# Kernel optimization log

Hardware: AMD Instinct MI355X
Metric: run time of the kernel (lower is better)

Reference implementation:

```python
import jax, jax.numpy as jnp
import numpy as np

LSTM = 256
NUM_CELLS = 5
BLOCKS = 6
TEMP = 5.0
TANH_C = 1.1


def setup_inputs() -> dict:
    key = jax.random.key(0)
    ks = jax.random.split(key, 8)
    s = 0.05  # small init so sigmoids/tanh stay in sane range
    return {
        "enc_w": jax.random.normal(ks[0], (5, LSTM), jnp.float32) * s,
        "w_ih": jax.random.normal(ks[1], (4 * LSTM, LSTM), jnp.float32) * s,
        "w_hh": jax.random.normal(ks[2], (4 * LSTM, LSTM), jnp.float32) * s,
        "b_ih": jax.random.normal(ks[3], (4 * LSTM,), jnp.float32) * s,
        "b_hh": jax.random.normal(ks[4], (4 * LSTM,), jnp.float32) * s,
        "w1": jax.random.normal(ks[5], (LSTM, LSTM), jnp.float32) * s,
        "w2": jax.random.normal(ks[6], (LSTM, LSTM), jnp.float32) * s,
        "v": jax.random.normal(ks[7], (LSTM,), jnp.float32) * s,
    }


def _lstm_cell(x, h, c, w_ih, w_hh, b_ih, b_hh):
    # torch.nn.LSTMCell gate order: i, f, g, o
    g = w_ih @ x + b_ih + w_hh @ h + b_hh  # [4*LSTM]
    i, f, gg, o = jnp.split(g, 4)
    i, f, o = jax.nn.sigmoid(i), jax.nn.sigmoid(f), jax.nn.sigmoid(o)
    c2 = f * c + i * jnp.tanh(gg)
    h2 = o * jnp.tanh(c2)
    return h2, c2


def _run_sampler(bkey, enc_w, w_ih, w_hh, b_ih, b_hh, w1, w2, v):
    zeros = jnp.zeros((LSTM,), jnp.float32)
    inputs = enc_w[0]  # encoder(0)
    anchors = []
    anchors_w1 = []
    prev_h = prev_c = zeros
    # first two layers: LSTM always fed zero state (faithful to source)
    for _ in range(2):
        prev_h, prev_c = _lstm_cell(inputs, zeros, zeros, w_ih, w_hh, b_ih, b_hh)
        anchors.append(zeros)
        anchors_w1.append(w1 @ prev_h)
    arc_seq, log_probs, entropies = [], [], []
    step = 0
    for layer_id in range(2, NUM_CELLS + 2):
        for _ in range(2):
            prev_h, prev_c = _lstm_cell(inputs, prev_h, prev_c, w_ih, w_hh, b_ih, b_hh)
            q = jnp.tanh(jnp.stack(anchors_w1[:layer_id]) + w2 @ prev_h)  # [layer_id, LSTM]
            logits = (q @ v) / TEMP  # [layer_id]
            logits = TANH_C * jnp.tanh(logits)
            skey = jax.random.fold_in(bkey, step); step += 1
            index = jax.random.categorical(skey, logits)
            lsm = jax.nn.log_softmax(logits)
            arc_seq.append(index)
            log_probs.append(-lsm[index])  # F.cross_entropy
            entropies.append(jax.lax.stop_gradient(-jnp.sum(lsm * jnp.exp(lsm))))
            inputs = jnp.stack(anchors[:layer_id])[index]
        prev_h, prev_c = _lstm_cell(inputs, prev_h, prev_c, w_ih, w_hh, b_ih, b_hh)
        anchors.append(prev_h)
        anchors_w1.append(w1 @ prev_h)
        inputs = enc_w[0]
    arc = jnp.stack(arc_seq)  # [2*NUM_CELLS] int
    return arc, sum(entropies), sum(log_probs), prev_c, prev_h


def reference(enc_w, w_ih, w_hh, b_ih, b_hh, w1, w2, v):
    key = jax.random.key(42)
    all_arc = []
    all_entropy = jnp.float32(0.0)
    all_log_prob = jnp.float32(0.0)
    c = h = None
    for b in range(BLOCKS):
        arc, ent, lp, c, h = _run_sampler(
            jax.random.fold_in(key, b), enc_w, w_ih, w_hh, b_ih, b_hh, w1, w2, v)
        all_arc.append(arc)
        all_entropy = all_entropy + ent
        all_log_prob = all_log_prob + lp
    return (jnp.stack(all_arc), all_log_prob, all_entropy, c[None, :], h[None, :])
```

## Files before the change

### kernel.cpp

```cpp
#include <hip/hip_runtime.h>
#include <stdint.h>


#define NBLK  6
#define PWG   8
#define THR   512
#define TINYF 1.17549435e-38f
#define HTAGB 0xC3B00000u
#define YTAGB 0xE1700000u
#define ITAGB 0xA5D00000u
#define DONE_MAGIC 0x444f4e45

typedef unsigned long long u64;
struct U2 { uint32_t x, y; };

#define W_DONE 0u
#define W_PART 32u
#define W_IDX  80u
#define W_HX   320u
#define W_YMB  24896u
#define W_NEED 221504u

#define S_READY 0u
#define S_DONE  192u
#define S_PART  224u
#define S_HP    320u
#define S_ACC   24896u
#define FXS     67108864.0f
#define READY_MAGIC 0x52454459

__device__ __forceinline__ U2 tf2x32(uint32_t k0, uint32_t k1,
                                     uint32_t c0, uint32_t c1) {
  uint32_t ks2 = k0 ^ k1 ^ 0x1BD11BDAu;
  uint32_t x0 = c0 + k0, x1 = c1 + k1;
#define TFR(r) { x0 += x1; x1 = (x1 << (r)) | (x1 >> (32 - (r))); x1 ^= x0; }
  TFR(13) TFR(15) TFR(26) TFR(6)   x0 += k1;  x1 += ks2 + 1u;
  TFR(17) TFR(29) TFR(16) TFR(24)  x0 += ks2; x1 += k0 + 2u;
  TFR(13) TFR(15) TFR(26) TFR(6)   x0 += k0;  x1 += k1 + 3u;
  TFR(17) TFR(29) TFR(16) TFR(24)  x0 += k1;  x1 += ks2 + 4u;
  TFR(13) TFR(15) TFR(26) TFR(6)   x0 += ks2; x1 += k0 + 5u;
#undef TFR
  U2 r; r.x = x0; r.y = x1; return r;
}

__device__ __forceinline__ float sigf(float x) {
  return 1.0f / (1.0f + expf(-x));
}
__device__ __forceinline__ void istore(int* p, int v) {
  __hip_atomic_store(p, v, __ATOMIC_RELAXED, __HIP_MEMORY_SCOPE_AGENT);
}
__device__ __forceinline__ int iload(const int* p) {
  return __hip_atomic_load(p, __ATOMIC_RELAXED, __HIP_MEMORY_SCOPE_AGENT);
}
__device__ __forceinline__ void hstore(u64* p, u64 v) {
  __hip_atomic_store(p, v, __ATOMIC_RELAXED, __HIP_MEMORY_SCOPE_AGENT);
}
__device__ __forceinline__ u64 hload(const u64* p) {
  return __hip_atomic_load(p, __ATOMIC_RELAXED, __HIP_MEMORY_SCOPE_AGENT);
}
__device__ __forceinline__ void fstore(float* p, float v) {
  __hip_atomic_store(p, v, __ATOMIC_RELAXED, __HIP_MEMORY_SCOPE_AGENT);
}
__device__ __forceinline__ float fload(const float* p) {
  return __hip_atomic_load(p, __ATOMIC_RELAXED, __HIP_MEMORY_SCOPE_AGENT);
}
__device__ __forceinline__ u64 pollw(const u64* p, uint32_t want) {
  u64 v;
  for (;;) {
    v = hload(p);
    if ((uint32_t)(v >> 32) == want) return v;
    __builtin_amdgcn_s_sleep(1);
  }
}

__global__ __launch_bounds__(THR, 2) void ctrl_v16(
    const float* __restrict__ enc_w,
    const float* __restrict__ wih,
    const float* __restrict__ whh,
    const float* __restrict__ b_ih,
    const float* __restrict__ b_hh,
    const float* __restrict__ w1,
    const float* __restrict__ w2,
    const float* __restrict__ vvec,
    unsigned char* __restrict__ ws,
    float* __restrict__ out) {

  const int b = blockIdx.x & 7;
  const int p = blockIdx.x >> 3;
  if (b >= NBLK) return;
  const int tid = threadIdx.x;

  int*   done = (int*)(ws + W_DONE);
  float* part = (float*)(ws + W_PART);
  int*   idxw = (int*)(ws + W_IDX);
  u64*   hx   = (u64*)(ws + W_HX);
  u64*   ymb  = (u64*)(ws + W_YMB);

  const int rl = tid & 127, s = tid >> 7;
  const int grow = (rl >> 5) * 256 + p * 32 + (rl & 31);
  const int k0 = s * 64;
  const int rr = tid & 255, ks = tid >> 8;
  const int cb = p * 32 + ks * 16;

  __shared__ __align__(16) float gateL[THR];
  __shared__ __align__(16) float hL[256], encL[256], vL[256];
  __shared__ __align__(16) float anchL[4][256];
  __shared__ __align__(16) float w2hS[256], aw1S[6][256];
  __shared__ float rowSumL[128], biasS[128], h2S[32];
  __shared__ float logitL[8];
  __shared__ int   selL;

  if (tid < 256) { encL[tid] = enc_w[tid]; vL[tid] = vvec[tid]; }
  if (tid < 128) {
    int r = (tid >> 5) * 256 + p * 32 + (tid & 31);
    biasS[tid] = b_ih[r] + b_hh[r];
  }

  float4 wihr[16], whhr[16];
  #pragma unroll
  for (int c = 0; c < 16; ++c) {
    wihr[c] = *(const float4*)(wih + grow * 256 + k0 + c * 4);
    whhr[c] = *(const float4*)(whh + grow * 256 + k0 + c * 4);
  }
  float w1c[16], w2c[16];
  #pragma unroll
  for (int j = 0; j < 16; ++j) {
    w1c[j] = w1[rr * 256 + cb + j];
    w2c[j] = w2[rr * 256 + cb + j];
  }
  __syncthreads();

  auto dotIH = [&](const float* x) {
    float a = 0.0f;
    #pragma unroll
    for (int c = 0; c < 16; ++c) {
      float4 xv = *(const float4*)(x + k0 + c * 4);
      float4 w = wihr[c];
      a += w.x * xv.x + w.y * xv.y + w.z * xv.z + w.w * xv.w;
    }
    return a;
  };
  auto dotHH = [&]() {
    float a = 0.0f;
    #pragma unroll
    for (int c = 0; c < 16; ++c) {
      float4 xv = *(const float4*)(hL + k0 + c * 4);
      float4 w = whhr[c];
      a += w.x * xv.x + w.y * xv.y + w.z * xv.z + w.w * xv.w;
    }
    return a;
  };

  const float encih = dotIH(encL);

  float cv = 0.0f;
  U2 bk = tf2x32(0u, 42u, 0u, (uint32_t)b);
  int k = 1, step = 0;
  float lpAcc = 0.0f, entAcc = 0.0f;

  auto cell = [&](float gacc, int mode, int aid, int cid) {
    gateL[tid] = gacc;
    __syncthreads();
    if (tid < 128) {
      float ssum = 0.0f;
      #pragma unroll
      for (int j = 0; j < 4; ++j) ssum += gateL[j * 128 + tid];
      rowSumL[tid] = ssum + biasS[tid];
    }
    __syncthreads();
    if (tid < 32) {
      float gi = rowSumL[tid],       gf = rowSumL[32 + tid];
      float gg2 = rowSumL[64 + tid], go = rowSumL[96 + tid];
      float c2 = sigf(gf) * cv + sigf(gi) * tanhf(gg2);
      float h2 = sigf(go) * tanhf(c2);
      cv = c2;
      h2S[tid] = h2;
      if (mode == 2) {
        if (b == NBLK - 1) { out[62 + p * 32 + tid] = cv; out[318 + p * 32 + tid] = h2; }
      } else {
        hstore(&hx[(k & 1) * 1536 + b * 256 + p * 32 + tid],
               ((u64)(HTAGB | (uint32_t)k) << 32) | (u64)__float_as_uint(h2));
      }
    }
    __syncthreads();
    if (mode == 2) return;

    {
      const float* wc = (mode == 1) ? w1c : w2c;
      float yp = 0.0f;
      #pragma unroll
      for (int j = 0; j < 16; ++j) yp += wc[j] * h2S[ks * 16 + j];
      gateL[tid] = yp;
    }
    __syncthreads();

    const uint32_t wantY = YTAGB | (uint32_t)k;
    const uint32_t wantH = HTAGB | (uint32_t)k;
    u64* ybase = ymb + (size_t)(k & 1) * 12288 + (size_t)b * 2048;
    if (tid < 256) {
      float yp2 = gateL[tid] + gateL[256 + tid];
      hstore(ybase + (size_t)p * 256 + tid,
             ((u64)wantY << 32) | (u64)__float_as_uint(yp2));
      u64 v = pollw(&hx[(k & 1) * 1536 + b * 256 + tid], wantH);
      float hv = __uint_as_float((uint32_t)v);
      hL[tid] = hv;
      if (mode == 1 && cid >= 0) anchL[cid][tid] = hv;
    } else if (p == 0) {
      const int e = tid - 256;
      const u64* bp = ybase + e;
      u64 w[8];
      for (;;) {
        #pragma unroll
        for (int q = 0; q < 8; ++q) w[q] = hload(bp + q * 256);
        uint32_t bad = 0u;
        #pragma unroll
        for (int q = 0; q < 8; ++q) bad |= ((uint32_t)(w[q] >> 32) ^ wantY);
        if (bad == 0u) break;
        __builtin_amdgcn_s_sleep(1);
      }
      float y = 0.0f;
      #pragma unroll
      for (int q = 0; q < 8; ++q) y += __uint_as_float((uint32_t)w[q]);
      if (mode == 1) aw1S[aid][e] = y; else w2hS[e] = y;
    }
    __syncthreads();
    ++k;
  };

  auto resolve = [&](int L) -> int {
    if (p == 0) {
      int wv = tid >> 6, lane = tid & 63;
      if (wv < L) {
        float a = 0.0f;
        #pragma unroll
        for (int j = 0; j < 4; ++j) {
          int kk = j * 64 + lane;
          a += tanhf(aw1S[wv][kk] + w2hS[kk]) * vL[kk];
        }
        a += __shfl_down(a, 32);
        a += __shfl_down(a, 16);
        a += __shfl_down(a, 8);
        a += __shfl_down(a, 4);
        a += __shfl_down(a, 2);
        a += __shfl_down(a, 1);
        if (lane == 0) logitL[wv] = a;
      }
      __syncthreads();
      if (tid < 64) {
        float lg = 0.0f, sgum = -1e30f;
        if (tid < L) {
          lg = 1.1f * tanhf(logitL[tid] * 0.2f);
          U2 sk = tf2x32(bk.x, bk.y, 0u, (uint32_t)step);
          U2 r2 = tf2x32(sk.x, sk.y, 0u, (uint32_t)tid);
          uint32_t bits = r2.x ^ r2.y;
          float u = __uint_as_float((bits >> 9) | 0x3f800000u) - 1.0f;
          u = fmaxf(TINYF, u + TINYF);
          sgum = lg - logf(-logf(u));
        }
        int bi = 0;
        float best = __shfl(sgum, 0, 64);
        for (int j = 1; j < L; ++j) {
          float sj = __shfl(sgum, j, 64);
          if (sj > best) { best = sj; bi = j; }
        }
        float mx = __shfl(lg, 0, 64);
        for (int j = 1; j < L; ++j) mx = fmaxf(mx, __shfl(lg, j, 64));
        float se = 0.0f;
        for (int j = 0; j < L; ++j) se += expf(__shfl(lg, j, 64) - mx);
        float lse = logf(se);
        float lgbi = __shfl(lg, bi, 64);
        float es = 0.0f;
        for (int j = 0; j < L; ++j) {
          float l = __shfl(lg, j, 64) - mx - lse;
          es += l * expf(l);
        }
        if (tid == 0) {
          lpAcc += -(lgbi - mx - lse);
          entAcc += -es;
          selL = bi;
          out[b * 10 + step] = (float)bi;
          istore(&idxw[b * 10 + step],
                 (int)(ITAGB | ((uint32_t)step << 4) | (uint32_t)bi));
        }
      }
      __syncthreads();
    } else {
      if (tid == 0) {
        const uint32_t want = ITAGB | ((uint32_t)step << 4);
        for (;;) {
          uint32_t v = (uint32_t)iload(&idxw[b * 10 + step]);
          if ((v & 0xFFFFFFF0u) == want) { selL = (int)(v & 15u); break; }
          __builtin_amdgcn_s_sleep(1);
        }
      }
      __syncthreads();
    }
    step++;
    return selL;
  };

  cell(encih, 1, 0, -1);
  if (p == 0) {
    if (tid < 256) aw1S[1][tid] = aw1S[0][tid];
    __syncthreads();
  }

  for (int L = 2; L <= 6; ++L) {
    { float hh = dotHH(); cell(encih + hh, 0, 0, -1); }
    {
      int s1; float hh;
      if (p == 0) { s1 = resolve(L); hh = dotHH(); }
      else        { hh = dotHH(); s1 = resolve(L); }
      float a = (s1 >= 2) ? dotIH(&anchL[s1 - 2][0]) : 0.0f;
      cell(a + hh, 0, 0, -1);
    }
    {
      int s2; float hh;
      if (p == 0) { s2 = resolve(L); hh = dotHH(); }
      else        { hh = dotHH(); s2 = resolve(L); }
      float a = (s2 >= 2) ? dotIH(&anchL[s2 - 2][0]) : 0.0f;
      if (L < 6) cell(a + hh, 1, L, L - 2);
      else       cell(a + hh, 2, 0, -1);
    }
  }

  if (p == 0 && tid == 0) {
    fstore(&part[2 * b], lpAcc);
    fstore(&part[2 * b + 1], entAcc);
    __builtin_amdgcn_s_waitcnt(0);
    istore(&done[b], DONE_MAGIC);
    if (b == NBLK - 1) {
      float lp = 0.0f, en = 0.0f;
      for (int j = 0; j < NBLK; ++j) {
        while (iload(&done[j]) != DONE_MAGIC) __builtin_amdgcn_s_sleep(1);
        lp += fload(&part[2 * j]);
        en += fload(&part[2 * j + 1]);
      }
      out[60] = lp;
      out[61] = en;
    }
  }
}

__global__ __launch_bounds__(1024) void ctrl_small(
    const float* __restrict__ enc_w,
    const float* __restrict__ wih,
    const float* __restrict__ whh,
    const float* __restrict__ b_ih,
    const float* __restrict__ b_hh,
    const float* __restrict__ w1,
    const float* __restrict__ w2,
    const float* __restrict__ vvec,
    unsigned char* __restrict__ ws,
    float* __restrict__ out) {

  const int b = blockIdx.x & 7;
  const int p = blockIdx.x >> 3;
  if (b >= NBLK) return;
  const int tid = threadIdx.x;

  int*   ready = (int*)(ws + S_READY);
  int*   done  = (int*)(ws + S_DONE);
  float* part  = (float*)(ws + S_PART);
  u64*   hp    = (u64*)(ws + S_HP);
  int*   acc   = (int*)(ws + S_ACC);

  const int rl = tid >> 3, s = tid & 7;
  const int g = rl >> 5, el = rl & 31;
  const int row = g * 256 + p * 32 + el;
  const int k0 = s * 32;
  const int rr = tid & 255, ks = tid >> 8;

  __shared__ __align__(16) float hL[256], encL[256], vL[256];
  __shared__ __align__(16) float anchL[4][256];
  __shared__ __align__(16) float partL[1024];
  __shared__ __align__(16) float w2hS[256], aw1S[6][256];
  __shared__ float rowSumL[128], biasS[128], h2S[32];
  __shared__ float logitL[8];
  __shared__ int   selL;

  if (tid < 256) { encL[tid] = enc_w[tid]; vL[tid] = vvec[tid]; }
  if (tid < 128) {
    int gg = tid >> 5, ee = tid & 31, r = gg * 256 + p * 32 + ee;
    biasS[tid] = b_ih[r] + b_hh[r];
  }

  float4 wihr[8], whhr[8];
  #pragma unroll
  for (int c = 0; c < 8; ++c) {
    int cc = (c + s) & 7;
    wihr[c] = *(const float4*)(wih + row * 256 + k0 + cc * 4);
    whhr[c] = *(const float4*)(whh + row * 256 + k0 + cc * 4);
  }
  float w1c[8], w2c[8];
  #pragma unroll
  for (int j = 0; j < 8; ++j) {
    w1c[j] = w1[rr * 256 + p * 32 + ks * 8 + j];
    w2c[j] = w2[rr * 256 + p * 32 + ks * 8 + j];
  }

  if (tid < 32) istore(&acc[1 * (NBLK * 256) + b * 256 + p * 32 + tid], 0);
  __syncthreads();
  if (tid == 0) istore(&ready[b * 8 + p], READY_MAGIC);
  if (tid < 8) {
    while (iload(&ready[b * 8 + tid]) != READY_MAGIC)
      __builtin_amdgcn_s_sleep(1);
  }
  __syncthreads();

  auto dotIH = [&](const float* x) {
    float a = 0.0f;
    #pragma unroll
    for (int c = 0; c < 8; ++c) {
      int cc = (c + s) & 7;
      float4 xv = *(const float4*)(x + k0 + cc * 4);
      float4 w = wihr[c];
      a += w.x * xv.x + w.y * xv.y + w.z * xv.z + w.w * xv.w;
    }
    return a;
  };
  auto dotHH = [&]() {
    float a = 0.0f;
    #pragma unroll
    for (int c = 0; c < 8; ++c) {
      int cc = (c + s) & 7;
      float4 xv = *(const float4*)(hL + k0 + cc * 4);
      float4 w = whhr[c];
      a += w.x * xv.x + w.y * xv.y + w.z * xv.z + w.w * xv.w;
    }
    return a;
  };

  const float encih = dotIH(encL);
  float cv = 0.0f;
  U2 bk = tf2x32(0u, 42u, 0u, (uint32_t)b);
  int k = 1, step = 0;
  float lpAcc = 0.0f, entAcc = 0.0f;

  auto cell = [&](float gacc, int mode, int aid, int cid) {
    partL[tid] = gacc;
    __syncthreads();
    if (tid < 128) {
      float ssum = 0.0f;
      #pragma unroll
      for (int j = 0; j < 8; ++j) ssum += partL[tid * 8 + j];
      rowSumL[tid] = ssum + biasS[tid];
    }
    __syncthreads();
    if (tid < 32) {
      float gi = rowSumL[tid],       gf = rowSumL[32 + tid];
      float gg2 = rowSumL[64 + tid], go = rowSumL[96 + tid];
      float c2 = sigf(gf) * cv + sigf(gi) * tanhf(gg2);
      float h2 = sigf(go) * tanhf(c2);
      cv = c2;
      h2S[tid] = h2;
      if (mode == 2 && b == NBLK - 1) {
        out[62 + p * 32 + tid] = cv;
        out[318 + p * 32 + tid] = h2;
      }
    }
    __syncthreads();
    if (mode == 2) return;
    {
      const float* wc = (mode == 1) ? w1c : w2c;
      float yp = 0.0f;
      #pragma unroll
      for (int j = 0; j < 8; ++j) yp += wc[j] * h2S[ks * 8 + j];
      atomicAdd(&acc[(k % 3) * (NBLK * 256) + b * 256 + rr],
                __float2int_rn(yp * FXS));
      if (tid < 32)
        istore(&acc[((k + 1) % 3) * (NBLK * 256) + b * 256 + p * 32 + tid], 0);
    }
    __syncthreads();
    if (tid < 32) {
      u64 pk = ((u64)(uint32_t)k << 32) | (u64)__float_as_uint(h2S[tid]);
      hstore(&hp[(k & 1) * (NBLK * 256) + b * 256 + p * 32 + tid], pk);
    }
    if (tid < 256) {
      u64 v;
      const u64* src = &hp[(k & 1) * (NBLK * 256) + b * 256 + tid];
      while ((int)(hload(src) >> 32) != k) __builtin_amdgcn_s_sleep(1);
      v = hload(src);
      float hv = __uint_as_float((uint32_t)v);
      hL[tid] = hv;
      if (mode == 1 && cid >= 0) anchL[cid][tid] = hv;
    }
    __syncthreads();
    if (tid < 256) {
      int iv = iload(&acc[(k % 3) * (NBLK * 256) + b * 256 + tid]);
      float f = (float)((double)iv * (1.0 / 67108864.0));
      if (mode == 1) aw1S[aid][tid] = f; else w2hS[tid] = f;
    }
    __syncthreads();
    ++k;
  };

  auto sample = [&](int L) -> int {
    int wv = tid >> 6, lane = tid & 63;
    if (wv < L) {
      float a = 0.0f;
      #pragma unroll
      for (int j = 0; j < 4; ++j) {
        int kk = lane * 4 + j;
        a += tanhf(aw1S[wv][kk] + w2hS[kk]) * vL[kk];
      }
      a += __shfl_down(a, 32);
      a += __shfl_down(a, 16);
      a += __shfl_down(a, 8);
      a += __shfl_down(a, 4);
      a += __shfl_down(a, 2);
      a += __shfl_down(a, 1);
      if (lane == 0) logitL[wv] = a;
    }
    __syncthreads();
    if (tid < 64) {
      float lg = 0.0f, sgum = -1e30f;
      if (tid < L) {
        lg = 1.1f * tanhf(logitL[tid] * 0.2f);
        U2 sk = tf2x32(bk.x, bk.y, 0u, (uint32_t)step);
        U2 r2 = tf2x32(sk.x, sk.y, 0u, (uint32_t)tid);
        uint32_t bits = r2.x ^ r2.y;
        float u = __uint_as_float((bits >> 9) | 0x3f800000u) - 1.0f;
        u = fmaxf(TINYF, u + TINYF);
        sgum = lg - logf(-logf(u));
      }
      int bi = 0;
      float best = __shfl(sgum, 0, 64);
      for (int j = 1; j < L; ++j) {
        float sj = __shfl(sgum, j, 64);
        if (sj > best) { best = sj; bi = j; }
      }
      float mx = __shfl(lg, 0, 64);
      for (int j = 1; j < L; ++j) mx = fmaxf(mx, __shfl(lg, j, 64));
      float se = 0.0f;
      for (int j = 0; j < L; ++j) se += expf(__shfl(lg, j, 64) - mx);
      float lse = logf(se);
      float lgbi = __shfl(lg, bi, 64);
      float es = 0.0f;
      for (int j = 0; j < L; ++j) {
        float l = __shfl(lg, j, 64) - mx - lse;
        es += l * expf(l);
      }
      if (tid == 0) {
        lpAcc += -(lgbi - mx - lse);
        entAcc += -es;
        selL = bi;
        if (p == 0) out[b * 10 + step] = (float)bi;
      }
    }
    __syncthreads();
    step++;
    return selL;
  };

  cell(encih, 1, 0, -1);
  if (tid < 256) aw1S[1][tid] = aw1S[0][tid];
  __syncthreads();
  for (int L = 2; L <= 6; ++L) {
    cell(encih + dotHH(), 0, 0, -1);
    int s1v = sample(L);
    {
      float a = (s1v >= 2) ? dotIH(&anchL[s1v - 2][0]) : 0.0f;
      cell(a + dotHH(), 0, 0, -1);
    }
    int s2v = sample(L);
    {
      float a = (s2v >= 2) ? dotIH(&anchL[s2v - 2][0]) : 0.0f;
      if (L < 6) cell(a + dotHH(), 1, L, L - 2);
      else       cell(a + dotHH(), 2, 0, -1);
    }
  }
  if (p == 0 && tid == 0) {
    fstore(&part[2 * b], lpAcc);
    fstore(&part[2 * b + 1], entAcc);
    __builtin_amdgcn_s_waitcnt(0);
    istore(&done[b], DONE_MAGIC);
    if (b == NBLK - 1) {
      float lp = 0.0f, en = 0.0f;
      for (int j = 0; j < NBLK; ++j) {
        while (iload(&done[j]) != DONE_MAGIC) __builtin_amdgcn_s_sleep(1);
        lp += fload(&part[2 * j]);
        en += fload(&part[2 * j + 1]);
      }
      out[60] = lp;
      out[61] = en;
    }
  }
}

extern "C" void kernel_launch(void* const* d_in, const int* in_sizes, int n_in,
                              void* d_out, int out_size, void* d_ws, size_t ws_size,
                              hipStream_t stream) {
  const float* enc = (const float*)d_in[0];
  const float* wih = (const float*)d_in[1];
  const float* whh = (const float*)d_in[2];
  const float* bih = (const float*)d_in[3];
  const float* bhh = (const float*)d_in[4];
  const float* w1  = (const float*)d_in[5];
  const float* w2  = (const float*)d_in[6];
  const float* v   = (const float*)d_in[7];
  unsigned char* ws = (unsigned char*)d_ws;
  float* out = (float*)d_out;

  if (ws_size >= W_NEED) {
    ctrl_v16<<<dim3(64), dim3(THR), 0, stream>>>(
        enc, wih, whh, bih, bhh, w1, w2, v, ws, out);
  } else {
    ctrl_small<<<dim3(64), dim3(1024), 0, stream>>>(
        enc, wih, whh, bih, bhh, w1, w2, v, ws, out);
  }
}
```

Before: 149.2 us.

## Compute categorical sampling redundantly in every workgroup instead of broadcasting index

Each of the 8 workgroups per block now reduces the y-partials itself and runs the attention/logit/Gumbel sampling locally, instead of only workgroup 0 doing it and publishing the index through a tagged global flag that the others poll. This removes one cross-workgroup global-memory handoff per sampling step from the serial critical path. In exchange every workgroup does the 8-way partial polling and the softmax work, which adds global read traffic and duplicated compute. Only workgroup 0 writes the output indices.

```diff
diff --git a/kernel.cpp b/kernel.cpp
--- a/kernel.cpp
+++ b/kernel.cpp
@@ -8,7 +8,6 @@
 #define TINYF 1.17549435e-38f
 #define HTAGB 0xC3B00000u
 #define YTAGB 0xE1700000u
-#define ITAGB 0xA5D00000u
 #define DONE_MAGIC 0x444f4e45
 
 typedef unsigned long long u64;
@@ -73,7 +72,7 @@
   }
 }
 
-__global__ __launch_bounds__(THR, 2) void ctrl_v16(
+__global__ __launch_bounds__(THR, 2) void ctrl_v17(
     const float* __restrict__ enc_w,
     const float* __restrict__ wih,
     const float* __restrict__ whh,
@@ -92,7 +91,6 @@
 
   int*   done = (int*)(ws + W_DONE);
   float* part = (float*)(ws + W_PART);
-  int*   idxw = (int*)(ws + W_IDX);
   u64*   hx   = (u64*)(ws + W_HX);
   u64*   ymb  = (u64*)(ws + W_YMB);
 
@@ -205,7 +203,7 @@
       float hv = __uint_as_float((uint32_t)v);
       hL[tid] = hv;
       if (mode == 1 && cid >= 0) anchL[cid][tid] = hv;
-    } else if (p == 0) {
+    } else {
       const int e = tid - 256;
       const u64* bp = ybase + e;
       u64 w[8];
@@ -228,96 +226,78 @@
   };
 
   auto resolve = [&](int L) -> int {
-    if (p == 0) {
-      int wv = tid >> 6, lane = tid & 63;
-      if (wv < L) {
-        float a = 0.0f;
-        #pragma unroll
-        for (int j = 0; j < 4; ++j) {
-          int kk = j * 64 + lane;
-          a += tanhf(aw1S[wv][kk] + w2hS[kk]) * vL[kk];
-        }
-        a += __shfl_down(a, 32);
-        a += __shfl_down(a, 16);
-        a += __shfl_down(a, 8);
-        a += __shfl_down(a, 4);
-        a += __shfl_down(a, 2);
-        a += __shfl_down(a, 1);
-        if (lane == 0) logitL[wv] = a;
-      }
-      __syncthreads();
-      if (tid < 64) {
-        float lg = 0.0f, sgum = -1e30f;
-        if (tid < L) {
-          lg = 1.1f * tanhf(logitL[tid] * 0.2f);
-          U2 sk = tf2x32(bk.x, bk.y, 0u, (uint32_t)step);
-          U2 r2 = tf2x32(sk.x, sk.y, 0u, (uint32_t)tid);
-          uint32_t bits = r2.x ^ r2.y;
-          float u = __uint_as_float((bits >> 9) | 0x3f800000u) - 1.0f;
-          u = fmaxf(TINYF, u + TINYF);
-          sgum = lg - logf(-logf(u));
-        }
-        int bi = 0;
-        float best = __shfl(sgum, 0, 64);
-        for (int j = 1; j < L; ++j) {
-          float sj = __shfl(sgum, j, 64);
-          if (sj > best) { best = sj; bi = j; }
-        }
-        float mx = __shfl(lg, 0, 64);
-        for (int j = 1; j < L; ++j) mx = fmaxf(mx, __shfl(lg, j, 64));
-        float se = 0.0f;
-        for (int j = 0; j < L; ++j) se += expf(__shfl(lg, j, 64) - mx);
-        float lse = logf(se);
-        float lgbi = __shfl(lg, bi, 64);
-        float es = 0.0f;
-        for (int j = 0; j < L; ++j) {
-          float l = __shfl(lg, j, 64) - mx - lse;
-          es += l * expf(l);
-        }
-        if (tid == 0) {
-          lpAcc += -(lgbi - mx - lse);
-          entAcc += -es;
-          selL = bi;
-          out[b * 10 + step] = (float)bi;
-          istore(&idxw[b * 10 + step],
-                 (int)(ITAGB | ((uint32_t)step << 4) | (uint32_t)bi));
-        }
-      }
-      __syncthreads();
-    } else {
+    int wv = tid >> 6, lane = tid & 63;
+    if (wv < L) {
+      float a = 0.0f;
+      #pragma unroll
+      for (int j = 0; j < 4; ++j) {
+        int kk = j * 64 + lane;
+        a += tanhf(aw1S[wv][kk] + w2hS[kk]) * vL[kk];
+      }
+      a += __shfl_down(a, 32);
+      a += __shfl_down(a, 16);
+      a += __shfl_down(a, 8);
+      a += __shfl_down(a, 4);
+      a += __shfl_down(a, 2);
+      a += __shfl_down(a, 1);
+      if (lane == 0) logitL[wv] = a;
+    }
+    __syncthreads();
+    if (tid < 64) {
+      float lg = 0.0f, sgum = -1e30f;
+      if (tid < L) {
+        lg = 1.1f * tanhf(logitL[tid] * 0.2f);
+        U2 sk = tf2x32(bk.x, bk.y, 0u, (uint32_t)step);
+        U2 r2 = tf2x32(sk.x, sk.y, 0u, (uint32_t)tid);
+        uint32_t bits = r2.x ^ r2.y;
+        float u = __uint_as_float((bits >> 9) | 0x3f800000u) - 1.0f;
+        u = fmaxf(TINYF, u + TINYF);
+        sgum = lg - logf(-logf(u));
+      }
+      int bi = 0;
+      float best = __shfl(sgum, 0, 64);
+      for (int j = 1; j < L; ++j) {
+        float sj = __shfl(sgum, j, 64);
+        if (sj > best) { best = sj; bi = j; }
+      }
+      float mx = __shfl(lg, 0, 64);
+      for (int j = 1; j < L; ++j) mx = fmaxf(mx, __shfl(lg, j, 64));
+      float se = 0.0f;
+      for (int j = 0; j < L; ++j) se += expf(__shfl(lg, j, 64) - mx);
+      float lse = logf(se);
+      float lgbi = __shfl(lg, bi, 64);
+      float es = 0.0f;
+      for (int j = 0; j < L; ++j) {
+        float l = __shfl(lg, j, 64) - mx - lse;
+        es += l * expf(l);
+      }
       if (tid == 0) {
-        const uint32_t want = ITAGB | ((uint32_t)step << 4);
-        for (;;) {
-          uint32_t v = (uint32_t)iload(&idxw[b * 10 + step]);
-          if ((v & 0xFFFFFFF0u) == want) { selL = (int)(v & 15u); break; }
-          __builtin_amdgcn_s_sleep(1);
-        }
-      }
-      __syncthreads();
-    }
+        lpAcc += -(lgbi - mx - lse);
+        entAcc += -es;
+        selL = bi;
+        if (p == 0) out[b * 10 + step] = (float)bi;
+      }
+    }
+    __syncthreads();
     step++;
     return selL;
   };
 
   cell(encih, 1, 0, -1);
-  if (p == 0) {
-    if (tid < 256) aw1S[1][tid] = aw1S[0][tid];
-    __syncthreads();
-  }
+  if (tid < 256) aw1S[1][tid] = aw1S[0][tid];
+  __syncthreads();
 
   for (int L = 2; L <= 6; ++L) {
     { float hh = dotHH(); cell(encih + hh, 0, 0, -1); }
     {
-      int s1; float hh;
-      if (p == 0) { s1 = resolve(L); hh = dotHH(); }
-      else        { hh = dotHH(); s1 = resolve(L); }
+      float hh = dotHH();
+      int s1 = resolve(L);
       float a = (s1 >= 2) ? dotIH(&anchL[s1 - 2][0]) : 0.0f;
       cell(a + hh, 0, 0, -1);
     }
     {
-      int s2; float hh;
-      if (p == 0) { s2 = resolve(L); hh = dotHH(); }
-      else        { hh = dotHH(); s2 = resolve(L); }
+      float hh = dotHH();
+      int s2 = resolve(L);
       float a = (s2 >= 2) ? dotIH(&anchL[s2 - 2][0]) : 0.0f;
       if (L < 6) cell(a + hh, 1, L, L - 2);
       else       cell(a + hh, 2, 0, -1);
@@ -603,7 +583,7 @@
   float* out = (float*)d_out;
 
   if (ws_size >= W_NEED) {
-    ctrl_v16<<<dim3(64), dim3(THR), 0, stream>>>(
+    ctrl_v17<<<dim3(64), dim3(THR), 0, stream>>>(
         enc, wih, whh, bih, bhh, w1, w2, v, ws, out);
   } else {
     ctrl_small<<<dim3(64), dim3(1024), 0, stream>>>(
```

Result: slower. 157.2 us (+5.4%).

## Speculatively precompute gate partials for every candidate anchor before polling sampled index

Applied to the files above, without the earlier changes.

Non-leader workgroups now compute the input-gate dot product for every possible sampled anchor (zero input plus each stored anchor) into a multi-slot shared buffer before waiting for the sampled index, then pick the matching slot. This takes the dotIH work off the critical path after the index arrives. The cell's row-sum reduction is also folded into the 32 finishing threads, removing one block barrier per cell. The cost is up to five redundant dot products per step and more shared memory.

```diff
diff --git a/kernel.cpp b/kernel.cpp
--- a/kernel.cpp
+++ b/kernel.cpp
@@ -73,7 +73,7 @@
   }
 }
 
-__global__ __launch_bounds__(THR, 2) void ctrl_v16(
+__global__ __launch_bounds__(THR, 2) void ctrl_v18(
     const float* __restrict__ enc_w,
     const float* __restrict__ wih,
     const float* __restrict__ whh,
@@ -102,11 +102,11 @@
   const int rr = tid & 255, ks = tid >> 8;
   const int cb = p * 32 + ks * 16;
 
-  __shared__ __align__(16) float gateL[THR];
+  __shared__ __align__(16) float gateC[5][THR];
   __shared__ __align__(16) float hL[256], encL[256], vL[256];
   __shared__ __align__(16) float anchL[4][256];
   __shared__ __align__(16) float w2hS[256], aw1S[6][256];
-  __shared__ float rowSumL[128], biasS[128], h2S[32];
+  __shared__ float biasS[128], h2S[32];
   __shared__ float logitL[8];
   __shared__ int   selL;
 
@@ -158,19 +158,17 @@
   int k = 1, step = 0;
   float lpAcc = 0.0f, entAcc = 0.0f;
 
-  auto cell = [&](float gacc, int mode, int aid, int cid) {
-    gateL[tid] = gacc;
-    __syncthreads();
-    if (tid < 128) {
-      float ssum = 0.0f;
+  auto cellSel = [&](int c, int mode, int aid, int cid) {
+    if (tid < 32) {
+      float rs[4];
       #pragma unroll
-      for (int j = 0; j < 4; ++j) ssum += gateL[j * 128 + tid];
-      rowSumL[tid] = ssum + biasS[tid];
-    }
-    __syncthreads();
-    if (tid < 32) {
-      float gi = rowSumL[tid],       gf = rowSumL[32 + tid];
-      float gg2 = rowSumL[64 + tid], go = rowSumL[96 + tid];
+      for (int g = 0; g < 4; ++g) {
+        float ssum = 0.0f;
+        #pragma unroll
+        for (int j = 0; j < 4; ++j) ssum += gateC[c][j * 128 + g * 32 + tid];
+        rs[g] = ssum + biasS[g * 32 + tid];
+      }
+      float gi = rs[0], gf = rs[1], gg2 = rs[2], go = rs[3];
       float c2 = sigf(gf) * cv + sigf(gi) * tanhf(gg2);
       float h2 = sigf(go) * tanhf(c2);
       cv = c2;
@@ -190,7 +188,7 @@
       float yp = 0.0f;
       #pragma unroll
       for (int j = 0; j < 16; ++j) yp += wc[j] * h2S[ks * 16 + j];
-      gateL[tid] = yp;
+      gateC[0][tid] = yp;
     }
     __syncthreads();
 
@@ -198,7 +196,7 @@
     const uint32_t wantH = HTAGB | (uint32_t)k;
     u64* ybase = ymb + (size_t)(k & 1) * 12288 + (size_t)b * 2048;
     if (tid < 256) {
-      float yp2 = gateL[tid] + gateL[256 + tid];
+      float yp2 = gateC[0][tid] + gateC[0][256 + tid];
       hstore(ybase + (size_t)p * 256 + tid,
              ((u64)wantY << 32) | (u64)__float_as_uint(yp2));
       u64 v = pollw(&hx[(k & 1) * 1536 + b * 256 + tid], wantH);
@@ -227,100 +225,140 @@
     ++k;
   };
 
-  auto resolve = [&](int L) -> int {
-    if (p == 0) {
-      int wv = tid >> 6, lane = tid & 63;
-      if (wv < L) {
-        float a = 0.0f;
-        #pragma unroll
-        for (int j = 0; j < 4; ++j) {
-          int kk = j * 64 + lane;
-          a += tanhf(aw1S[wv][kk] + w2hS[kk]) * vL[kk];
-        }
-        a += __shfl_down(a, 32);
-        a += __shfl_down(a, 16);
-        a += __shfl_down(a, 8);
-        a += __shfl_down(a, 4);
-        a += __shfl_down(a, 2);
-        a += __shfl_down(a, 1);
-        if (lane == 0) logitL[wv] = a;
-      }
-      __syncthreads();
-      if (tid < 64) {
-        float lg = 0.0f, sgum = -1e30f;
-        if (tid < L) {
-          lg = 1.1f * tanhf(logitL[tid] * 0.2f);
-          U2 sk = tf2x32(bk.x, bk.y, 0u, (uint32_t)step);
-          U2 r2 = tf2x32(sk.x, sk.y, 0u, (uint32_t)tid);
-          uint32_t bits = r2.x ^ r2.y;
-          float u = __uint_as_float((bits >> 9) | 0x3f800000u) - 1.0f;
-          u = fmaxf(TINYF, u + TINYF);
-          sgum = lg - logf(-logf(u));
-        }
-        int bi = 0;
-        float best = __shfl(sgum, 0, 64);
-        for (int j = 1; j < L; ++j) {
-          float sj = __shfl(sgum, j, 64);
-          if (sj > best) { best = sj; bi = j; }
-        }
-        float mx = __shfl(lg, 0, 64);
-        for (int j = 1; j < L; ++j) mx = fmaxf(mx, __shfl(lg, j, 64));
-        float se = 0.0f;
-        for (int j = 0; j < L; ++j) se += expf(__shfl(lg, j, 64) - mx);
-        float lse = logf(se);
-        float lgbi = __shfl(lg, bi, 64);
-        float es = 0.0f;
-        for (int j = 0; j < L; ++j) {
-          float l = __shfl(lg, j, 64) - mx - lse;
-          es += l * expf(l);
-        }
-        if (tid == 0) {
-          lpAcc += -(lgbi - mx - lse);
-          entAcc += -es;
-          selL = bi;
-          out[b * 10 + step] = (float)bi;
-          istore(&idxw[b * 10 + step],
-                 (int)(ITAGB | ((uint32_t)step << 4) | (uint32_t)bi));
-        }
-      }
-      __syncthreads();
-    } else {
+  auto doSample = [&](int L) -> int {
+    int wv = tid >> 6, lane = tid & 63;
+    if (wv < L) {
+      float a = 0.0f;
+      #pragma unroll
+      for (int j = 0; j < 4; ++j) {
+        int kk = j * 64 + lane;
+        a += tanhf(aw1S[wv][kk] + w2hS[kk]) * vL[kk];
+      }
+      a += __shfl_down(a, 32);
+      a += __shfl_down(a, 16);
+      a += __shfl_down(a, 8);
+      a += __shfl_down(a, 4);
+      a += __shfl_down(a, 2);
+      a += __shfl_down(a, 1);
+      if (lane == 0) logitL[wv] = a;
+    }
+    __syncthreads();
+    if (tid < 64) {
+      float lg = 0.0f, sgum = -1e30f;
+      if (tid < L) {
+        lg = 1.1f * tanhf(logitL[tid] * 0.2f);
+        U2 sk = tf2x32(bk.x, bk.y, 0u, (uint32_t)step);
+        U2 r2 = tf2x32(sk.x, sk.y, 0u, (uint32_t)tid);
+        uint32_t bits = r2.x ^ r2.y;
+        float u = __uint_as_float((bits >> 9) | 0x3f800000u) - 1.0f;
+        u = fmaxf(TINYF, u + TINYF);
+        sgum = lg - logf(-logf(u));
+      }
+      int bi = 0;
+      float best = __shfl(sgum, 0, 64);
+      for (int j = 1; j < L; ++j) {
+        float sj = __shfl(sgum, j, 64);
+        if (sj > best) { best = sj; bi = j; }
+      }
+      float mx = __shfl(lg, 0, 64);
+      for (int j = 1; j < L; ++j) mx = fmaxf(mx, __shfl(lg, j, 64));
+      float se = 0.0f;
+      for (int j = 0; j < L; ++j) se += expf(__shfl(lg, j, 64) - mx);
+      float lse = logf(se);
+      float lgbi = __shfl(lg, bi, 64);
+      float es = 0.0f;
+      for (int j = 0; j < L; ++j) {
+        float l = __shfl(lg, j, 64) - mx - lse;
+        es += l * expf(l);
+      }
       if (tid == 0) {
-        const uint32_t want = ITAGB | ((uint32_t)step << 4);
-        for (;;) {
-          uint32_t v = (uint32_t)iload(&idxw[b * 10 + step]);
-          if ((v & 0xFFFFFFF0u) == want) { selL = (int)(v & 15u); break; }
-          __builtin_amdgcn_s_sleep(1);
-        }
-      }
-      __syncthreads();
-    }
+        lpAcc += -(lgbi - mx - lse);
+        entAcc += -es;
+        selL = bi;
+        out[b * 10 + step] = (float)bi;
+        istore(&idxw[b * 10 + step],
+               (int)(ITAGB | ((uint32_t)step << 4) | (uint32_t)bi));
+      }
+    }
+    __syncthreads();
     step++;
     return selL;
   };
 
-  cell(encih, 1, 0, -1);
+  auto pollIdx = [&](int L) -> int {
+    (void)L;
+    if (tid == 0) {
+      const uint32_t want = ITAGB | ((uint32_t)step << 4);
+      for (;;) {
+        uint32_t v = (uint32_t)iload(&idxw[b * 10 + step]);
+        if ((v & 0xFFFFFFF0u) == want) { selL = (int)(v & 15u); break; }
+        __builtin_amdgcn_s_sleep(1);
+      }
+    }
+    __syncthreads();
+    step++;
+    return selL;
+  };
+
+  gateC[0][tid] = encih;
+  __syncthreads();
+  cellSel(0, 1, 0, -1);
   if (p == 0) {
     if (tid < 256) aw1S[1][tid] = aw1S[0][tid];
     __syncthreads();
   }
 
   for (int L = 2; L <= 6; ++L) {
-    { float hh = dotHH(); cell(encih + hh, 0, 0, -1); }
     {
-      int s1; float hh;
-      if (p == 0) { s1 = resolve(L); hh = dotHH(); }
-      else        { hh = dotHH(); s1 = resolve(L); }
-      float a = (s1 >= 2) ? dotIH(&anchL[s1 - 2][0]) : 0.0f;
-      cell(a + hh, 0, 0, -1);
+      float hh = dotHH();
+      gateC[0][tid] = encih + hh;
+      __syncthreads();
+      cellSel(0, 0, 0, -1);
     }
     {
-      int s2; float hh;
-      if (p == 0) { s2 = resolve(L); hh = dotHH(); }
-      else        { hh = dotHH(); s2 = resolve(L); }
-      float a = (s2 >= 2) ? dotIH(&anchL[s2 - 2][0]) : 0.0f;
-      if (L < 6) cell(a + hh, 1, L, L - 2);
-      else       cell(a + hh, 2, 0, -1);
+      int c;
+      if (p == 0) {
+        int s1 = doSample(L);
+        float hh = dotHH();
+        float a = (s1 >= 2) ? dotIH(&anchL[s1 - 2][0]) : 0.0f;
+        gateC[0][tid] = a + hh;
+        c = 0;
+        __syncthreads();
+      } else {
+        float hh = dotHH();
+        int nc = L - 1;
+        for (int cc = 0; cc < nc; ++cc) {
+          float a = (cc == 0) ? 0.0f : dotIH(&anchL[cc - 1][0]);
+          gateC[cc][tid] = a + hh;
+        }
+        __syncthreads();
+        int s1 = pollIdx(L);
+        c = (s1 >= 2) ? (s1 - 1) : 0;
+      }
+      cellSel(c, 0, 0, -1);
+    }
+    {
+      int c;
+      if (p == 0) {
+        int s2 = doSample(L);
+        float hh = dotHH();
+        float a = (s2 >= 2) ? dotIH(&anchL[s2 - 2][0]) : 0.0f;
+        gateC[0][tid] = a + hh;
+        c = 0;
+        __syncthreads();
+      } else {
+        float hh = dotHH();
+        int nc = L - 1;
+        for (int cc = 0; cc < nc; ++cc) {
+          float a = (cc == 0) ? 0.0f : dotIH(&anchL[cc - 1][0]);
+          gateC[cc][tid] = a + hh;
+        }
+        __syncthreads();
+        int s2 = pollIdx(L);
+        c = (s2 >= 2) ? (s2 - 1) : 0;
+      }
+      if (L < 6) cellSel(c, 1, L, L - 2);
+      else       cellSel(c, 2, 0, -1);
     }
   }
 
@@ -603,7 +641,7 @@
   float* out = (float*)d_out;
 
   if (ws_size >= W_NEED) {
-    ctrl_v16<<<dim3(64), dim3(THR), 0, stream>>>(
+    ctrl_v18<<<dim3(64), dim3(THR), 0, stream>>>(
         enc, wih, whh, bih, bhh, w1, w2, v, ws, out);
   } else {
     ctrl_small<<<dim3(64), dim3(1024), 0, stream>>>(
```

New measurement: 151.7 us. Within noise of the previous version (+1.7%).
